# Optimization experiments

Measured on AMD Instinct MI355X. Metric: run time of the kernel, lower is better.

## Reference

```python
import jax, jax.numpy as jnp
import numpy as np
import math

H, E, HD = 12, 768, 64   # heads, embed_dim, per-head hidden
B, S, L = 8, 512, 512    # batch, dec len, enc len
EPS = 1e-12


def layer_norm(x, w, b):
    u = jnp.mean(x, axis=-1, keepdims=True)
    s = jnp.mean((x - u) ** 2, axis=-1, keepdims=True)
    return w * (x - u) / jnp.sqrt(s + EPS) + b


def gelu(x):
    return x * 0.5 * (1.0 + jax.lax.erf(x / math.sqrt(2.0)))


def attention(k, q, w_k, w_q, pw, pb, mask):
    # k:[b,kl,E] q:[b,ql,E] w_k/w_q:[H,E,HD] mask broadcastable to [b,H,ql,kl]
    kx = jnp.einsum('ble,hed->bhld', k, w_k)
    qx = jnp.einsum('bqe,hed->bhqd', q, w_q)
    score = jnp.einsum('bhqd,bhkd->bhqk', qx, kx) / math.sqrt(HD)
    score = jnp.where(mask, score, jnp.asarray(-1e4, score.dtype))
    attn = jax.nn.softmax(score, axis=-1)
    out = jnp.einsum('bhqk,bhkd->bhqd', attn, kx)  # values are kx (as in source)
    b_, h, ql, d = out.shape
    out = out.transpose(0, 2, 1, 3).reshape(b_, ql, h * d)
    return out @ pw + pb


def setup_inputs() -> dict:
    key = jax.random.key(0)
    ks = jax.random.split(key, 16)
    xav = lambda k, shp, fan: jax.random.normal(k, shp, jnp.float32) * math.sqrt(2.0 / fan)
    inp = {
        'X': jax.random.normal(ks[0], (B, S, E), jnp.float32),
        'enc_outputs': jax.random.normal(ks[1], (B, L, E), jnp.float32),
        'enc_valid_lens': jax.random.randint(ks[2], (B,), 1, L + 1, jnp.int32),
        'w_kx1': xav(ks[3], (H, E, HD), E + HD),
        'w_qx1': xav(ks[4], (H, E, HD), E + HD),
        'proj1_w': xav(ks[5], (H * HD, E), 2 * E),
        'proj1_b': jnp.zeros((E,), jnp.float32),
        'ln1_w': jnp.ones((E,), jnp.float32),
        'ln1_b': jnp.zeros((E,), jnp.float32),
        'w_kx2': xav(ks[6], (H, E, HD), E + HD),
        'w_qx2': xav(ks[7], (H, E, HD), E + HD),
        'proj2_w': xav(ks[8], (H * HD, E), 2 * E),
        'proj2_b': jnp.zeros((E,), jnp.float32),
        'ln2_w': jnp.ones((E,), jnp.float32),
        'ln2_b': jnp.zeros((E,), jnp.float32),
        'ffn_w1': xav(ks[9], (E, E), 2 * E),
        'ffn_b1': jnp.zeros((E,), jnp.float32),
        'ffn_w2': xav(ks[10], (E, E), 2 * E),
        'ffn_b2': jnp.zeros((E,), jnp.float32),
        'ln3_w': jnp.ones((E,), jnp.float32),
        'ln3_b': jnp.zeros((E,), jnp.float32),
    }
    return inp


def reference(X, enc_outputs, enc_valid_lens,
              w_kx1, w_qx1, proj1_w, proj1_b, ln1_w, ln1_b,
              w_kx2, w_qx2, proj2_w, proj2_b, ln2_w, ln2_b,
              ffn_w1, ffn_b1, ffn_w2, ffn_b2, ln3_w, ln3_b):
    s = X.shape[1]
    # training path: dec_valid_lens is 2D -> causal mask in Attention
    causal = jnp.tril(jnp.ones((s, s), dtype=bool))[None, None]          # [1,1,s,s]
    X2 = attention(X, X, w_kx1, w_qx1, proj1_w, proj1_b, causal)
    Y = layer_norm(X2 + X, ln1_w, ln1_b)
    # cross mask: key padding from enc_valid_lens (1D branch)
    kl = enc_outputs.shape[1]
    pad = (jnp.arange(kl)[None] < enc_valid_lens[:, None])[:, None, None]  # [b,1,1,kl]
    Y2 = attention(enc_outputs, Y, w_kx2, w_qx2, proj2_w, proj2_b, pad)
    Z = layer_norm(Y2 + Y, ln2_w, ln2_b)
    F = gelu(Z @ ffn_w1 + ffn_b1) @ ffn_w2 + ffn_b2
    return layer_norm(F + Z, ln3_w, ln3_b)
```

## Files before the change

kernel.cpp:

```cpp
#include <hip/hip_runtime.h>
#include <hip/hip_bf16.h>

typedef __hip_bfloat16 bf16;
typedef __attribute__((ext_vector_type(8))) short s8v;
typedef __attribute__((ext_vector_type(4))) short s4v;
typedef __attribute__((ext_vector_type(4))) float f4v;

#define H_ 12
#define E_ 768
#define HD_ 64
#define B_ 8
#define S_ 512
#define M_ 4096

struct P9 { const void* s[8]; bf16* d[8]; const void* vs[10]; bf16* vd[10]; };

typedef __attribute__((address_space(3))) void lds_void;
typedef const __attribute__((address_space(1))) void g_void;

__device__ __forceinline__ void async_copy16(const bf16* g, short* l) {
    __builtin_amdgcn_global_load_lds((g_void*)g, (lds_void*)l, 16, 0, 0);
}

__device__ __forceinline__ float sh2f(short v) {
    unsigned int u = ((unsigned int)(unsigned short)v) << 16;
    return __uint_as_float(u);
}

__device__ __forceinline__ short f2sh(float v) {
    bf16 b = __float2bfloat16(v);
    return *(short*)&b;
}

__device__ __forceinline__ int detect_fp32(const unsigned int* __restrict__ Xh,
                                           int tid, int* scratch) {
    unsigned e = (Xh[tid] >> 7) & 0xFFu;
    int good = (e >= 100u && e <= 141u) ? 1 : 0;
    #pragma unroll
    for (int off = 1; off < 64; off <<= 1) good += __shfl_xor(good, off);
    if ((tid & 63) == 0) scratch[tid >> 6] = good;
    __syncthreads();
    int total = scratch[0] + scratch[1] + scratch[2] + scratch[3];
    return (total <= 154) ? 1 : 0;
}

__device__ __forceinline__ bf16 ldcvt(const void* s, int i, int fp32) {
    return fp32 ? __float2bfloat16(((const float*)s)[i]) : ((const bf16*)s)[i];
}

__global__ __launch_bounds__(256) void prep_kernel(const void* X, const void* enc,
                                                   bf16* Xc, bf16* ENCc,
                                                   P9 p) {
    __shared__ int dsc[4];
    __shared__ float t[64][65];
    const int tid = threadIdx.x;
    const int fp32 = detect_fp32((const unsigned int*)X, tid, dsc);
    const int id = blockIdx.x;

    if (id < 6144) {
        const void* s = (id < 3072) ? X : enc;
        bf16* d = (id < 3072) ? Xc : ENCc;
        int cid = (id < 3072) ? id : id - 3072;
        int i = (cid * 256 + tid) * 4;
        if (fp32) {
            float4 v = *(const float4*)((const float*)s + i);
            bf16 a = __float2bfloat16(v.x), b = __float2bfloat16(v.y),
                 c = __float2bfloat16(v.z), e = __float2bfloat16(v.w);
            s4v o = { *(short*)&a, *(short*)&b, *(short*)&c, *(short*)&e };
            *(s4v*)(d + i) = o;
        } else {
            *(s4v*)(d + i) = *(const s4v*)((const bf16*)s + i);
        }
        return;
    }

    int id2 = id - 6144;
    const int z = id2 / 144;
    const int rem = id2 % 144;
    const int bx = rem % 12, by = rem / 12;

    if (z == 8) {
        int vid = by * 12 + bx;
        if (vid < 10) {
            const void* s = p.vs[vid];
            bf16* d = p.vd[vid];
            for (int i = tid; i < E_; i += 256) d[i] = ldcvt(s, i, fp32);
        }
        return;
    }
    const int c = tid & 63, r0 = tid >> 6;
    if (z < 4) {
        const void* s = p.s[z];
        bf16* d = p.d[z];
        const int e0 = bx * 64, h = by;
        #pragma unroll
        for (int j = 0; j < 16; ++j) {
            int r = r0 * 16 + j;
            int idx = (h * E_ + e0 + r) * HD_ + c;
            t[r][c] = fp32 ? ((const float*)s)[idx] : __bfloat162float(((const bf16*)s)[idx]);
        }
        __syncthreads();
        #pragma unroll
        for (int j = 0; j < 16; ++j) {
            int r = r0 * 16 + j;
            d[(size_t)(h * 64 + r) * E_ + e0 + c] = __float2bfloat16(t[c][r]);
        }
    } else {
        const void* s = p.s[z];
        bf16* d = p.d[z];
        const int k0 = bx * 64, n0 = by * 64;
        #pragma unroll
        for (int j = 0; j < 16; ++j) {
            int r = r0 * 16 + j;
            int idx = (k0 + r) * E_ + n0 + c;
            t[r][c] = fp32 ? ((const float*)s)[idx] : __bfloat162float(((const bf16*)s)[idx]);
        }
        __syncthreads();
        #pragma unroll
        for (int j = 0; j < 16; ++j) {
            int r = r0 * 16 + j;
            d[(size_t)(n0 + r) * E_ + k0 + c] = __float2bfloat16(t[c][r]);
        }
    }
}

template <int EPI>
__global__ __launch_bounds__(256, 4) void gemm3(const bf16* __restrict__ A,
                                                const bf16* __restrict__ Bt,
                                                bf16* __restrict__ C,
                                                const bf16* __restrict__ bias,
                                                const bf16* __restrict__ res) {
    __shared__ short As[64 * 128];
    __shared__ short Bs[64 * 128];
    const int bm = blockIdx.x, bn = blockIdx.y;
    const int tid = threadIdx.x;
    const int w = tid >> 6, l = tid & 63;
    const int wr = (w >> 1) * 32, wc = (w & 1) * 32;
    const int lc = l & 15, quad = l >> 4;
    const int srA = l >> 4, slot = l & 15;

    f4v acc[2][2] = {};

    for (int k0 = 0; k0 < E_; k0 += 128) {
        #pragma unroll
        for (int c = 0; c < 4; ++c) {
            int seg = w * 4 + c;
            int row = seg * 4 + srA;
            int kc = (slot ^ (row & 15)) * 8;
            async_copy16(A + (size_t)(bm * 64 + row) * E_ + k0 + kc, &As[seg * 512]);
            async_copy16(Bt + (size_t)(bn * 64 + row) * E_ + k0 + kc, &Bs[seg * 512]);
        }
        __syncthreads();

        #pragma unroll
        for (int kk = 0; kk < 4; ++kk) {
            s8v a[2], b[2];
            #pragma unroll
            for (int t = 0; t < 2; ++t) {
                int ar = wr + t * 16 + lc;
                a[t] = *(const s8v*)&As[ar * 128 + (((kk * 4 + quad) ^ (ar & 15)) * 8)];
                int bc = wc + t * 16 + lc;
                b[t] = *(const s8v*)&Bs[bc * 128 + (((kk * 4 + quad) ^ (bc & 15)) * 8)];
            }
            acc[0][0] = __builtin_amdgcn_mfma_f32_16x16x32_bf16(a[0], b[0], acc[0][0], 0, 0, 0);
            acc[0][1] = __builtin_amdgcn_mfma_f32_16x16x32_bf16(a[0], b[1], acc[0][1], 0, 0, 0);
            acc[1][0] = __builtin_amdgcn_mfma_f32_16x16x32_bf16(a[1], b[0], acc[1][0], 0, 0, 0);
            acc[1][1] = __builtin_amdgcn_mfma_f32_16x16x32_bf16(a[1], b[1], acc[1][1], 0, 0, 0);
        }
        __syncthreads();
    }

    #pragma unroll
    for (int mt = 0; mt < 2; ++mt)
        #pragma unroll
        for (int nt = 0; nt < 2; ++nt)
            #pragma unroll
            for (int i = 0; i < 4; ++i) {
                int row = bm * 64 + wr + mt * 16 + quad * 4 + i;
                int col = bn * 64 + wc + nt * 16 + lc;
                float v = acc[mt][nt][i];
                if (EPI == 1)
                    v += __bfloat162float(bias[col]) + __bfloat162float(res[(size_t)row * E_ + col]);
                if (EPI == 2) {
                    v += __bfloat162float(bias[col]);
                    v = 0.5f * v * (1.0f + erff(v * 0.70710678118654752f));
                }
                C[(size_t)row * E_ + col] = __float2bfloat16(v);
            }
}

__global__ __launch_bounds__(256, 4) void gemm3q(const bf16* __restrict__ Xc,
                                                 const bf16* __restrict__ ENCc,
                                                 const bf16* __restrict__ Bt,
                                                 bf16* __restrict__ K1,
                                                 bf16* __restrict__ Q1,
                                                 bf16* __restrict__ K2,
                                                 bf16* __restrict__ KT1,
                                                 bf16* __restrict__ KT2) {
    __shared__ short sm[16384];
    short* As = sm;
    short* Bs = sm + 8192;
    const int bm = blockIdx.x, bn = blockIdx.y;
    const int tid = threadIdx.x;
    const int w = tid >> 6, l = tid & 63;
    const int wr = (w >> 1) * 32, wc = (w & 1) * 32;
    const int lc = l & 15, quad = l >> 4;
    const int srA = l >> 4, slot = l & 15;

    const bf16* A = (bn >= 24) ? ENCc : Xc;

    f4v acc[2][2] = {};

    for (int k0 = 0; k0 < E_; k0 += 128) {
        #pragma unroll
        for (int c = 0; c < 4; ++c) {
            int seg = w * 4 + c;
            int row = seg * 4 + srA;
            int kc = (slot ^ (row & 15)) * 8;
            async_copy16(A + (size_t)(bm * 64 + row) * E_ + k0 + kc, &As[seg * 512]);
            async_copy16(Bt + (size_t)(bn * 64 + row) * E_ + k0 + kc, &Bs[seg * 512]);
        }
        __syncthreads();

        #pragma unroll
        for (int kk = 0; kk < 4; ++kk) {
            s8v a[2], b[2];
            #pragma unroll
            for (int t = 0; t < 2; ++t) {
                int ar = wr + t * 16 + lc;
                a[t] = *(const s8v*)&As[ar * 128 + (((kk * 4 + quad) ^ (ar & 15)) * 8)];
                int bc = wc + t * 16 + lc;
                b[t] = *(const s8v*)&Bs[bc * 128 + (((kk * 4 + quad) ^ (bc & 15)) * 8)];
            }
            acc[0][0] = __builtin_amdgcn_mfma_f32_16x16x32_bf16(a[0], b[0], acc[0][0], 0, 0, 0);
            acc[0][1] = __builtin_amdgcn_mfma_f32_16x16x32_bf16(a[0], b[1], acc[0][1], 0, 0, 0);
            acc[1][0] = __builtin_amdgcn_mfma_f32_16x16x32_bf16(a[1], b[0], acc[1][0], 0, 0, 0);
            acc[1][1] = __builtin_amdgcn_mfma_f32_16x16x32_bf16(a[1], b[1], acc[1][1], 0, 0, 0);
        }
        __syncthreads();
    }

    const int band = (bn < 12) ? 0 : (bn < 24) ? 1 : 2;
    const int nb = bn - band * 12;
    bf16* C = (band == 0) ? K1 : (band == 1) ? Q1 : K2;

    #pragma unroll
    for (int mt = 0; mt < 2; ++mt)
        #pragma unroll
        for (int nt = 0; nt < 2; ++nt)
            #pragma unroll
            for (int i = 0; i < 4; ++i) {
                int row = bm * 64 + wr + mt * 16 + quad * 4 + i;
                int col = nb * 64 + wc + nt * 16 + lc;
                C[(size_t)row * E_ + col] = __float2bfloat16(acc[mt][nt][i]);
            }

    if (band != 1) {
        bf16* KT = (band == 0) ? KT1 : KT2;
        #pragma unroll
        for (int mt = 0; mt < 2; ++mt)
            #pragma unroll
            for (int nt = 0; nt < 2; ++nt)
                #pragma unroll
                for (int i = 0; i < 4; ++i) {
                    int srow = wr + mt * 16 + quad * 4 + i;
                    int d = wc + nt * 16 + lc;
                    sm[d * 72 + srow] = f2sh(acc[mt][nt][i]);
                }
        __syncthreads();
        const int drow = tid >> 2, c0 = (tid & 3) * 16;
        s8v o0 = *(const s8v*)&sm[drow * 72 + c0];
        s8v o1 = *(const s8v*)&sm[drow * 72 + c0 + 8];
        const int b = bm >> 3, s0 = (bm & 7) * 64;
        bf16* dp = KT + ((size_t)((b * H_ + nb) * 64 + drow) * S_) + s0 + c0;
        *(s8v*)dp = o0;
        *(s8v*)(dp + 8) = o1;
    }
}

template <bool CAUSAL, bool INLQ>
__global__ __launch_bounds__(256) void attn_kernel(const bf16* __restrict__ Q,
                                                   const bf16* __restrict__ Wq,
                                                   const bf16* __restrict__ Kx,
                                                   const bf16* __restrict__ KT,
                                                   bf16* __restrict__ O,
                                                   const int* __restrict__ vlen) {
    __shared__ short qs[64 * 64];
    __shared__ short ks[64 * 64];
    __shared__ short kts[80 * 64];
    __shared__ short ps[64 * 72];

    const int bh = blockIdx.x, qt = blockIdx.y;
    const int h = bh % H_, b = bh / H_;
    const int tid = threadIdx.x, w = tid >> 6, l = tid & 63;
    const int lr = (l >> 4) * 4, lc = l & 15, quad = l >> 4;
    const int srA = l >> 3, slot = l & 7;
    const int kc = (slot ^ srA) * 8;
    const int rq = w * 16 + lc;

    {
        int r = 64 + (tid >> 4);
        int c4 = (tid & 15) * 4;
        s4v v = {};
        if (r == 64) { v[0] = 0x3F80; v[1] = 0x3F80; v[2] = 0x3F80; v[3] = 0x3F80; }
        *(s4v*)&kts[r * 64 + c4] = v;
    }

    if (INLQ) {
        const int wr = (w >> 1) * 32, wc = (w & 1) * 32;
        const bf16* Arow = Q + (size_t)(b * S_ + qt * 64) * E_;
        const bf16* Brow = Wq + (size_t)(h * 64) * E_;
        f4v qacc[2][2] = {};
        for (int k0 = 0; k0 < E_; k0 += 64) {
            #pragma unroll
            for (int c = 0; c < 2; ++c) {
                int seg = w * 2 + c;
                int row = seg * 8 + srA;
                async_copy16(Arow + (size_t)row * E_ + k0 + kc, &ks[seg * 512]);
                async_copy16(Brow + (size_t)row * E_ + k0 + kc, &kts[seg * 512]);
            }
            __syncthreads();
            #pragma unroll
            for (int kk = 0; kk < 2; ++kk) {
                s8v a[2], bb[2];
                #pragma unroll
                for (int t = 0; t < 2; ++t) {
                    int ar = wr + t * 16 + lc;
                    a[t] = *(const s8v*)&ks[ar * 64 + (((kk * 4 + quad) ^ (ar & 7)) * 8)];
                    int bc = wc + t * 16 + lc;
                    bb[t] = *(const s8v*)&kts[bc * 64 + (((kk * 4 + quad) ^ (bc & 7)) * 8)];
                }
                qacc[0][0] = __builtin_amdgcn_mfma_f32_16x16x32_bf16(a[0], bb[0], qacc[0][0], 0, 0, 0);
                qacc[0][1] = __builtin_amdgcn_mfma_f32_16x16x32_bf16(a[0], bb[1], qacc[0][1], 0, 0, 0);
                qacc[1][0] = __builtin_amdgcn_mfma_f32_16x16x32_bf16(a[1], bb[0], qacc[1][0], 0, 0, 0);
                qacc[1][1] = __builtin_amdgcn_mfma_f32_16x16x32_bf16(a[1], bb[1], qacc[1][1], 0, 0, 0);
            }
            __syncthreads();
        }
        #pragma unroll
        for (int mt = 0; mt < 2; ++mt)
            #pragma unroll
            for (int nt = 0; nt < 2; ++nt)
                #pragma unroll
                for (int i = 0; i < 4; ++i) {
                    int row = wr + mt * 16 + quad * 4 + i;
                    int d = wc + nt * 16 + lc;
                    qs[row * 64 + (((d >> 3) ^ (row & 7)) * 8) + (d & 7)] = f2sh(qacc[mt][nt][i]);
                }
        __syncthreads();
    } else {
        #pragma unroll
        for (int c = 0; c < 2; ++c) {
            int seg = w * 2 + c;
            int row = seg * 8 + srA;
            async_copy16(Q + ((size_t)(b * S_ + qt * 64 + row) * H_ + h) * HD_ + kc, &qs[seg * 512]);
        }
    }

    const int valid = CAUSAL ? S_ : vlen[b];
    const int kmax = CAUSAL ? (qt + 1) : ((valid + 63) >> 6);

    f4v o_acc[5] = {};
    s8v aq0, aq1;

    for (int kt = 0; kt < kmax; ++kt) {
        #pragma unroll
        for (int c = 0; c < 2; ++c) {
            int seg = w * 2 + c;
            int row = seg * 8 + srA;
            async_copy16(Kx + ((size_t)(b * S_ + kt * 64 + row) * H_ + h) * HD_ + kc, &ks[seg * 512]);
            async_copy16(KT + (size_t)(bh * 64 + row) * S_ + kt * 64 + kc, &kts[seg * 512]);
        }
        __syncthreads();

        if (kt == 0) {
            aq0 = *(const s8v*)&qs[rq * 64 + ((quad ^ (rq & 7)) * 8)];
            aq1 = *(const s8v*)&qs[rq * 64 + (((4 + quad) ^ (rq & 7)) * 8)];
        }

        f4v sacc[4] = {};
        #pragma unroll
        for (int nt = 0; nt < 4; nt++) {
            int rk = nt * 16 + lc;
            s8v bk0 = *(const s8v*)&ks[rk * 64 + ((quad ^ (rk & 7)) * 8)];
            s8v bk1 = *(const s8v*)&ks[rk * 64 + (((4 + quad) ^ (rk & 7)) * 8)];
            sacc[nt] = __builtin_amdgcn_mfma_f32_16x16x32_bf16(aq0, bk0, sacc[nt], 0, 0, 0);
            sacc[nt] = __builtin_amdgcn_mfma_f32_16x16x32_bf16(aq1, bk1, sacc[nt], 0, 0, 0);
        }

        #pragma unroll
        for (int i = 0; i < 4; i++) {
            int qabs = qt * 64 + w * 16 + lr + i;
            #pragma unroll
            for (int nt = 0; nt < 4; nt++) {
                int kabs = kt * 64 + nt * 16 + lc;
                bool ok = CAUSAL ? (kabs <= qabs) : (kabs < valid);
                float sv = ok ? fminf(sacc[nt][i] * 0.125f - 20.0f, 0.0f) : -1.0e4f;
                ps[(w * 16 + lr + i) * 72 + nt * 16 + lc] = f2sh(__expf(sv));
            }
        }

        s8v ap0 = *(const s8v*)&ps[rq * 72 + quad * 8];
        s8v ap1 = *(const s8v*)&ps[rq * 72 + 32 + quad * 8];
        #pragma unroll
        for (int dt = 0; dt < 5; dt++) {
            int rd = dt * 16 + lc;
            s8v bv0 = *(const s8v*)&kts[rd * 64 + ((quad ^ (rd & 7)) * 8)];
            s8v bv1 = *(const s8v*)&kts[rd * 64 + (((4 + quad) ^ (rd & 7)) * 8)];
            o_acc[dt] = __builtin_amdgcn_mfma_f32_16x16x32_bf16(ap0, bv0, o_acc[dt], 0, 0, 0);
            o_acc[dt] = __builtin_amdgcn_mfma_f32_16x16x32_bf16(ap1, bv1, o_acc[dt], 0, 0, 0);
        }
        if (kt + 1 < kmax) __syncthreads();
    }

    float li[4];
    #pragma unroll
    for (int i = 0; i < 4; i++) li[i] = __shfl(o_acc[4][i], (l & 48));

    #pragma unroll
    for (int dt = 0; dt < 4; dt++)
        #pragma unroll
        for (int i = 0; i < 4; i++) {
            int q = qt * 64 + w * 16 + lr + i;
            int d = dt * 16 + lc;
            float v = o_acc[dt][i] / li[i];
            O[((size_t)(b * S_ + q) * H_ + h) * HD_ + d] = __float2bfloat16(v);
        }
}

__global__ __launch_bounds__(256) void ln2_kernel(const bf16* __restrict__ X,
                                                  const bf16* __restrict__ wv,
                                                  const bf16* __restrict__ bv,
                                                  bf16* __restrict__ outb,
                                                  float* __restrict__ outf,
                                                  const unsigned int* __restrict__ Xhead) {
    __shared__ int dsc[4];
    int f32out = 0;
    if (outf != nullptr)
        f32out = detect_fp32(Xhead, threadIdx.x, dsc);
    const int row = blockIdx.x * 4 + (threadIdx.x >> 6);
    const int l = threadIdx.x & 63;
    const bf16* xr = X + (size_t)row * E_;
    s8v v8 = *(const s8v*)(xr + l * 8);
    s4v v4 = *(const s4v*)(xr + 512 + l * 4);
    float x[12];
    #pragma unroll
    for (int j = 0; j < 8; ++j) x[j] = sh2f(v8[j]);
    #pragma unroll
    for (int j = 0; j < 4; ++j) x[8 + j] = sh2f(v4[j]);
    float s = 0.f, ss = 0.f;
    #pragma unroll
    for (int j = 0; j < 12; ++j) { s += x[j]; ss += x[j] * x[j]; }
    #pragma unroll
    for (int off = 1; off < 64; off <<= 1) {
        s += __shfl_xor(s, off);
        ss += __shfl_xor(ss, off);
    }
    float mu = s * (1.0f / E_);
    float var = ss * (1.0f / E_) - mu * mu;
    float rstd = rsqrtf(fmaxf(var, 0.0f) + 1e-12f);
    #pragma unroll
    for (int j = 0; j < 12; ++j) {
        int c = (j < 8) ? (l * 8 + j) : (512 + l * 4 + (j - 8));
        float v = (x[j] - mu) * rstd * __bfloat162float(wv[c]) + __bfloat162float(bv[c]);
        if (f32out) outf[(size_t)row * E_ + c] = v;
        else        outb[(size_t)row * E_ + c] = __float2bfloat16(v);
    }
}

extern "C" void kernel_launch(void* const* d_in, const int* in_sizes, int n_in,
                              void* d_out, int out_size, void* d_ws, size_t ws_size,
                              hipStream_t stream) {
    const void* X = d_in[0];
    const void* enc = d_in[1];
    const int* vlen = (const int*)d_in[2];

    char* ws = (char*)d_ws;
    bf16* vecs = (bf16*)(ws + 256);
    char* wbase = ws + 16384;
    const size_t WSZ = (size_t)E_ * E_ * sizeof(bf16);
    bf16* wk1 = (bf16*)(wbase + 0 * WSZ);
    bf16* wq1 = (bf16*)(wbase + 1 * WSZ);
    bf16* wk2 = (bf16*)(wbase + 2 * WSZ);
    bf16* wq2 = (bf16*)(wbase + 3 * WSZ);
    bf16* p1t = (bf16*)(wbase + 4 * WSZ);
    bf16* p2t = (bf16*)(wbase + 5 * WSZ);
    bf16* f1t = (bf16*)(wbase + 6 * WSZ);
    bf16* f2t = (bf16*)(wbase + 7 * WSZ);
    const size_t ASZ = (size_t)M_ * E_ * sizeof(bf16);
    char* abase = wbase + 8 * WSZ;
    bf16* Xc   = (bf16*)(abase + 0 * ASZ);
    bf16* ENCc = (bf16*)(abase + 1 * ASZ);
    bf16* A0  = (bf16*)(abase + 2 * ASZ);
    bf16* A1  = (bf16*)(abase + 3 * ASZ);
    bf16* A2  = (bf16*)(abase + 4 * ASZ);
    bf16* A3  = (bf16*)(abase + 5 * ASZ);
    bf16* A4  = (bf16*)(abase + 6 * ASZ);
    bf16* A5  = (bf16*)(abase + 7 * ASZ);
    bf16* KT1 = (bf16*)(abase + 8 * ASZ);
    bf16* KT2 = (bf16*)(abase + 9 * ASZ);

    bf16* bias1 = vecs + 0 * E_;
    bf16* lw1   = vecs + 1 * E_;
    bf16* lb1   = vecs + 2 * E_;
    bf16* bias2 = vecs + 3 * E_;
    bf16* lw2   = vecs + 4 * E_;
    bf16* lb2   = vecs + 5 * E_;
    bf16* fb1   = vecs + 6 * E_;
    bf16* fb2   = vecs + 7 * E_;
    bf16* lw3   = vecs + 8 * E_;
    bf16* lb3   = vecs + 9 * E_;

    P9 rp;
    rp.s[0] = d_in[3];  rp.d[0] = wk1;
    rp.s[1] = d_in[4];  rp.d[1] = wq1;
    rp.s[2] = d_in[9];  rp.d[2] = wk2;
    rp.s[3] = d_in[10]; rp.d[3] = wq2;
    rp.s[4] = d_in[5];  rp.d[4] = p1t;
    rp.s[5] = d_in[11]; rp.d[5] = p2t;
    rp.s[6] = d_in[15]; rp.d[6] = f1t;
    rp.s[7] = d_in[17]; rp.d[7] = f2t;
    rp.vs[0] = d_in[6];  rp.vd[0] = bias1;
    rp.vs[1] = d_in[7];  rp.vd[1] = lw1;
    rp.vs[2] = d_in[8];  rp.vd[2] = lb1;
    rp.vs[3] = d_in[12]; rp.vd[3] = bias2;
    rp.vs[4] = d_in[13]; rp.vd[4] = lw2;
    rp.vs[5] = d_in[14]; rp.vd[5] = lb2;
    rp.vs[6] = d_in[16]; rp.vd[6] = fb1;
    rp.vs[7] = d_in[18]; rp.vd[7] = fb2;
    rp.vs[8] = d_in[19]; rp.vd[8] = lw3;
    rp.vs[9] = d_in[20]; rp.vd[9] = lb3;

    prep_kernel<<<7440, 256, 0, stream>>>(X, enc, Xc, ENCc, rp);

    gemm3q<<<dim3(64, 36), 256, 0, stream>>>(Xc, ENCc, wk1, A0, A1, A4, KT1, KT2);

    attn_kernel<true, false><<<dim3(96, 8), 256, 0, stream>>>(A1, nullptr, A0, KT1, A2, nullptr);
    gemm3<1><<<dim3(64, 12), 256, 0, stream>>>(A2, p1t, A3, bias1, Xc);
    ln2_kernel<<<M_ / 4, 256, 0, stream>>>(A3, lw1, lb1, A5, nullptr, nullptr);

    attn_kernel<false, true><<<dim3(96, 8), 256, 0, stream>>>(A5, wq2, A4, KT2, A2, vlen);
    gemm3<1><<<dim3(64, 12), 256, 0, stream>>>(A2, p2t, A3, bias2, A5);
    ln2_kernel<<<M_ / 4, 256, 0, stream>>>(A3, lw2, lb2, A0, nullptr, nullptr);

    gemm3<2><<<dim3(64, 12), 256, 0, stream>>>(A0, f1t, A1, fb1, nullptr);
    gemm3<1><<<dim3(64, 12), 256, 0, stream>>>(A1, f2t, A2, fb2, A0);
    ln2_kernel<<<M_ / 4, 256, 0, stream>>>(A2, lw3, lb3, (bf16*)d_out, (float*)d_out,
                                           (const unsigned int*)X);
}
```

Before: 261.0 us.

## Fuse LayerNorm into residual GEMM via last-block atomic counter

Replaces the three separate LayerNorm kernels with a fused GEMM variant. After writing its output tile, each block increments a per-row-tile atomic counter, and the last of the 12 column blocks for that row stripe normalises the 64 full rows. Counters are zeroed in the prep kernel. This removes three kernel launches and a separate pass. In exchange, the LayerNorm runs on only 64 blocks with serialised row loops at the tail, and it adds fence and atomic overhead.

```diff
diff --git a/kernel.cpp b/kernel.cpp
--- a/kernel.cpp
+++ b/kernel.cpp
@@ -13,7 +13,7 @@
 #define S_ 512
 #define M_ 4096
 
-struct P9 { const void* s[8]; bf16* d[8]; const void* vs[10]; bf16* vd[10]; };
+struct P9 { const void* s[8]; bf16* d[8]; const void* vs[10]; bf16* vd[10]; int* cnt; };
 
 typedef __attribute__((address_space(3))) void lds_void;
 typedef const __attribute__((address_space(1))) void g_void;
@@ -85,6 +85,8 @@
             const void* s = p.vs[vid];
             bf16* d = p.vd[vid];
             for (int i = tid; i < E_; i += 256) d[i] = ldcvt(s, i, fp32);
+        } else if (vid == 10) {
+            if (tid < 192) p.cnt[tid] = 0;
         }
         return;
     }
@@ -187,6 +189,116 @@
                 }
                 C[(size_t)row * E_ + col] = __float2bfloat16(v);
             }
+}
+
+template <int DET>
+__global__ __launch_bounds__(256, 4) void gemm3ln(const bf16* __restrict__ A,
+                                                  const bf16* __restrict__ Bt,
+                                                  bf16* __restrict__ C,
+                                                  const bf16* __restrict__ bias,
+                                                  const bf16* __restrict__ res,
+                                                  const bf16* __restrict__ lnw,
+                                                  const bf16* __restrict__ lnb,
+                                                  bf16* __restrict__ outb,
+                                                  float* __restrict__ outf,
+                                                  int* __restrict__ cnt,
+                                                  const unsigned int* __restrict__ Xhead) {
+    __shared__ short As[64 * 128];
+    __shared__ short Bs[64 * 128];
+    __shared__ int dsc[4];
+    __shared__ int lastFlag;
+    const int bm = blockIdx.x, bn = blockIdx.y;
+    const int tid = threadIdx.x;
+    const int w = tid >> 6, l = tid & 63;
+    const int wr = (w >> 1) * 32, wc = (w & 1) * 32;
+    const int lc = l & 15, quad = l >> 4;
+    const int srA = l >> 4, slot = l & 15;
+
+    f4v acc[2][2] = {};
+
+    for (int k0 = 0; k0 < E_; k0 += 128) {
+        #pragma unroll
+        for (int c = 0; c < 4; ++c) {
+            int seg = w * 4 + c;
+            int row = seg * 4 + srA;
+            int kc = (slot ^ (row & 15)) * 8;
+            async_copy16(A + (size_t)(bm * 64 + row) * E_ + k0 + kc, &As[seg * 512]);
+            async_copy16(Bt + (size_t)(bn * 64 + row) * E_ + k0 + kc, &Bs[seg * 512]);
+        }
+        __syncthreads();
+
+        #pragma unroll
+        for (int kk = 0; kk < 4; ++kk) {
+            s8v a[2], b[2];
+            #pragma unroll
+            for (int t = 0; t < 2; ++t) {
+                int ar = wr + t * 16 + lc;
+                a[t] = *(const s8v*)&As[ar * 128 + (((kk * 4 + quad) ^ (ar & 15)) * 8)];
+                int bc = wc + t * 16 + lc;
+                b[t] = *(const s8v*)&Bs[bc * 128 + (((kk * 4 + quad) ^ (bc & 15)) * 8)];
+            }
+            acc[0][0] = __builtin_amdgcn_mfma_f32_16x16x32_bf16(a[0], b[0], acc[0][0], 0, 0, 0);
+            acc[0][1] = __builtin_amdgcn_mfma_f32_16x16x32_bf16(a[0], b[1], acc[0][1], 0, 0, 0);
+            acc[1][0] = __builtin_amdgcn_mfma_f32_16x16x32_bf16(a[1], b[0], acc[1][0], 0, 0, 0);
+            acc[1][1] = __builtin_amdgcn_mfma_f32_16x16x32_bf16(a[1], b[1], acc[1][1], 0, 0, 0);
+        }
+        __syncthreads();
+    }
+
+    #pragma unroll
+    for (int mt = 0; mt < 2; ++mt)
+        #pragma unroll
+        for (int nt = 0; nt < 2; ++nt)
+            #pragma unroll
+            for (int i = 0; i < 4; ++i) {
+                int row = bm * 64 + wr + mt * 16 + quad * 4 + i;
+                int col = bn * 64 + wc + nt * 16 + lc;
+                float v = acc[mt][nt][i]
+                        + __bfloat162float(bias[col])
+                        + __bfloat162float(res[(size_t)row * E_ + col]);
+                C[(size_t)row * E_ + col] = __float2bfloat16(v);
+            }
+
+    __threadfence();
+    __syncthreads();
+    if (tid == 0) lastFlag = (atomicAdd(cnt + bm, 1) == 11);
+    __syncthreads();
+    if (!lastFlag) return;
+    __threadfence();
+
+    int f32o = 0;
+    if (DET) f32o = detect_fp32(Xhead, tid, dsc);
+
+    #pragma unroll 1
+    for (int rr = 0; rr < 16; ++rr) {
+        int row = bm * 64 + w * 16 + rr;
+        const bf16* xr = C + (size_t)row * E_;
+        s8v v8 = *(const s8v*)(xr + l * 8);
+        s4v v4 = *(const s4v*)(xr + 512 + l * 4);
+        float x[12];
+        #pragma unroll
+        for (int j = 0; j < 8; ++j) x[j] = sh2f(v8[j]);
+        #pragma unroll
+        for (int j = 0; j < 4; ++j) x[8 + j] = sh2f(v4[j]);
+        float s = 0.f, ss = 0.f;
+        #pragma unroll
+        for (int j = 0; j < 12; ++j) { s += x[j]; ss += x[j] * x[j]; }
+        #pragma unroll
+        for (int off = 1; off < 64; off <<= 1) {
+            s += __shfl_xor(s, off);
+            ss += __shfl_xor(ss, off);
+        }
+        float mu = s * (1.0f / E_);
+        float var = ss * (1.0f / E_) - mu * mu;
+        float rstd = rsqrtf(fmaxf(var, 0.0f) + 1e-12f);
+        #pragma unroll
+        for (int j = 0; j < 12; ++j) {
+            int c = (j < 8) ? (l * 8 + j) : (512 + l * 4 + (j - 8));
+            float v = (x[j] - mu) * rstd * __bfloat162float(lnw[c]) + __bfloat162float(lnb[c]);
+            if (DET && f32o) outf[(size_t)row * E_ + c] = v;
+            else             outb[(size_t)row * E_ + c] = __float2bfloat16(v);
+        }
+    }
 }
 
 __global__ __launch_bounds__(256, 4) void gemm3q(const bf16* __restrict__ Xc,
@@ -428,46 +540,6 @@
         }
 }
 
-__global__ __launch_bounds__(256) void ln2_kernel(const bf16* __restrict__ X,
-                                                  const bf16* __restrict__ wv,
-                                                  const bf16* __restrict__ bv,
-                                                  bf16* __restrict__ outb,
-                                                  float* __restrict__ outf,
-                                                  const unsigned int* __restrict__ Xhead) {
-    __shared__ int dsc[4];
-    int f32out = 0;
-    if (outf != nullptr)
-        f32out = detect_fp32(Xhead, threadIdx.x, dsc);
-    const int row = blockIdx.x * 4 + (threadIdx.x >> 6);
-    const int l = threadIdx.x & 63;
-    const bf16* xr = X + (size_t)row * E_;
-    s8v v8 = *(const s8v*)(xr + l * 8);
-    s4v v4 = *(const s4v*)(xr + 512 + l * 4);
-    float x[12];
-    #pragma unroll
-    for (int j = 0; j < 8; ++j) x[j] = sh2f(v8[j]);
-    #pragma unroll
-    for (int j = 0; j < 4; ++j) x[8 + j] = sh2f(v4[j]);
-    float s = 0.f, ss = 0.f;
-    #pragma unroll
-    for (int j = 0; j < 12; ++j) { s += x[j]; ss += x[j] * x[j]; }
-    #pragma unroll
-    for (int off = 1; off < 64; off <<= 1) {
-        s += __shfl_xor(s, off);
-        ss += __shfl_xor(ss, off);
-    }
-    float mu = s * (1.0f / E_);
-    float var = ss * (1.0f / E_) - mu * mu;
-    float rstd = rsqrtf(fmaxf(var, 0.0f) + 1e-12f);
-    #pragma unroll
-    for (int j = 0; j < 12; ++j) {
-        int c = (j < 8) ? (l * 8 + j) : (512 + l * 4 + (j - 8));
-        float v = (x[j] - mu) * rstd * __bfloat162float(wv[c]) + __bfloat162float(bv[c]);
-        if (f32out) outf[(size_t)row * E_ + c] = v;
-        else        outb[(size_t)row * E_ + c] = __float2bfloat16(v);
-    }
-}
-
 extern "C" void kernel_launch(void* const* d_in, const int* in_sizes, int n_in,
                               void* d_out, int out_size, void* d_ws, size_t ws_size,
                               hipStream_t stream) {
@@ -476,7 +548,8 @@
     const int* vlen = (const int*)d_in[2];
 
     char* ws = (char*)d_ws;
-    bf16* vecs = (bf16*)(ws + 256);
+    int* cnt = (int*)ws;
+    bf16* vecs = (bf16*)(ws + 1024);
     char* wbase = ws + 16384;
     const size_t WSZ = (size_t)E_ * E_ * sizeof(bf16);
     bf16* wk1 = (bf16*)(wbase + 0 * WSZ);
@@ -530,21 +603,22 @@
     rp.vs[7] = d_in[18]; rp.vd[7] = fb2;
     rp.vs[8] = d_in[19]; rp.vd[8] = lw3;
     rp.vs[9] = d_in[20]; rp.vd[9] = lb3;
+    rp.cnt = cnt;
 
     prep_kernel<<<7440, 256, 0, stream>>>(X, enc, Xc, ENCc, rp);
 
     gemm3q<<<dim3(64, 36), 256, 0, stream>>>(Xc, ENCc, wk1, A0, A1, A4, KT1, KT2);
 
     attn_kernel<true, false><<<dim3(96, 8), 256, 0, stream>>>(A1, nullptr, A0, KT1, A2, nullptr);
-    gemm3<1><<<dim3(64, 12), 256, 0, stream>>>(A2, p1t, A3, bias1, Xc);
-    ln2_kernel<<<M_ / 4, 256, 0, stream>>>(A3, lw1, lb1, A5, nullptr, nullptr);
+    gemm3ln<0><<<dim3(64, 12), 256, 0, stream>>>(A2, p1t, A3, bias1, Xc,
+                                                 lw1, lb1, A5, nullptr, cnt + 0, nullptr);
 
     attn_kernel<false, true><<<dim3(96, 8), 256, 0, stream>>>(A5, wq2, A4, KT2, A2, vlen);
-    gemm3<1><<<dim3(64, 12), 256, 0, stream>>>(A2, p2t, A3, bias2, A5);
-    ln2_kernel<<<M_ / 4, 256, 0, stream>>>(A3, lw2, lb2, A0, nullptr, nullptr);
+    gemm3ln<0><<<dim3(64, 12), 256, 0, stream>>>(A2, p2t, A3, bias2, A5,
+                                                 lw2, lb2, A0, nullptr, cnt + 64, nullptr);
 
     gemm3<2><<<dim3(64, 12), 256, 0, stream>>>(A0, f1t, A1, fb1, nullptr);
-    gemm3<1><<<dim3(64, 12), 256, 0, stream>>>(A1, f2t, A2, fb2, A0);
-    ln2_kernel<<<M_ / 4, 256, 0, stream>>>(A2, lw3, lb3, (bf16*)d_out, (float*)d_out,
-                                           (const unsigned int*)X);
-}
+    gemm3ln<1><<<dim3(64, 12), 256, 0, stream>>>(A1, f2t, A2, fb2, A0,
+                                                 lw3, lb3, (bf16*)d_out, (float*)d_out,
+                                                 cnt + 128, (const unsigned int*)X);
+}
```

Result: slower. 564.5 us (+116.3%).

## Double-buffer QKV projection GEMM and rebalance causal attention block schedule

Applied to the files above, without the earlier changes.

The fused K/Q projection GEMM now uses 64-wide K tiles in two LDS buffers, issuing async loads for the next tile while MFMAs run on the current one, instead of loading a 128-wide tile then waiting. The causal attention kernel remaps block IDs through a lookup table that interleaves long and short query tiles across heads, so concurrently resident blocks carry more even causal work. This adds table logic and depends on the grid shape matching the 96x8 layout.

```diff
diff --git a/kernel.cpp b/kernel.cpp
--- a/kernel.cpp
+++ b/kernel.cpp
@@ -198,39 +198,52 @@
                                                  bf16* __restrict__ KT1,
                                                  bf16* __restrict__ KT2) {
     __shared__ short sm[16384];
-    short* As = sm;
-    short* Bs = sm + 8192;
     const int bm = blockIdx.x, bn = blockIdx.y;
     const int tid = threadIdx.x;
     const int w = tid >> 6, l = tid & 63;
     const int wr = (w >> 1) * 32, wc = (w & 1) * 32;
     const int lc = l & 15, quad = l >> 4;
-    const int srA = l >> 4, slot = l & 15;
+    const int srA = l >> 3, slot = l & 7;
+    const int kc = (slot ^ srA) * 8;
 
     const bf16* A = (bn >= 24) ? ENCc : Xc;
+    const bf16* Ab = A + (size_t)(bm * 64) * E_;
+    const bf16* Bb = Bt + (size_t)(bn * 64) * E_;
 
     f4v acc[2][2] = {};
 
-    for (int k0 = 0; k0 < E_; k0 += 128) {
-        #pragma unroll
-        for (int c = 0; c < 4; ++c) {
-            int seg = w * 4 + c;
-            int row = seg * 4 + srA;
-            int kc = (slot ^ (row & 15)) * 8;
-            async_copy16(A + (size_t)(bm * 64 + row) * E_ + k0 + kc, &As[seg * 512]);
-            async_copy16(Bt + (size_t)(bn * 64 + row) * E_ + k0 + kc, &Bs[seg * 512]);
-        }
-        __syncthreads();
-
-        #pragma unroll
-        for (int kk = 0; kk < 4; ++kk) {
+    #pragma unroll
+    for (int c = 0; c < 2; ++c) {
+        int seg = w * 2 + c;
+        int row = seg * 8 + srA;
+        async_copy16(Ab + (size_t)row * E_ + kc, &sm[seg * 512]);
+        async_copy16(Bb + (size_t)row * E_ + kc, &sm[8192 + seg * 512]);
+    }
+    __syncthreads();
+
+    #pragma unroll
+    for (int kt = 0; kt < 12; ++kt) {
+        const int cur = (kt & 1) * 4096;
+        if (kt < 11) {
+            const int nxt = ((kt + 1) & 1) * 4096;
+            const int k0 = (kt + 1) * 64;
+            #pragma unroll
+            for (int c = 0; c < 2; ++c) {
+                int seg = w * 2 + c;
+                int row = seg * 8 + srA;
+                async_copy16(Ab + (size_t)row * E_ + k0 + kc, &sm[nxt + seg * 512]);
+                async_copy16(Bb + (size_t)row * E_ + k0 + kc, &sm[8192 + nxt + seg * 512]);
+            }
+        }
+        #pragma unroll
+        for (int kk = 0; kk < 2; ++kk) {
             s8v a[2], b[2];
             #pragma unroll
             for (int t = 0; t < 2; ++t) {
                 int ar = wr + t * 16 + lc;
-                a[t] = *(const s8v*)&As[ar * 128 + (((kk * 4 + quad) ^ (ar & 15)) * 8)];
+                a[t] = *(const s8v*)&sm[cur + ar * 64 + (((kk * 4 + quad) ^ (ar & 7)) * 8)];
                 int bc = wc + t * 16 + lc;
-                b[t] = *(const s8v*)&Bs[bc * 128 + (((kk * 4 + quad) ^ (bc & 15)) * 8)];
+                b[t] = *(const s8v*)&sm[8192 + cur + bc * 64 + (((kk * 4 + quad) ^ (bc & 7)) * 8)];
             }
             acc[0][0] = __builtin_amdgcn_mfma_f32_16x16x32_bf16(a[0], b[0], acc[0][0], 0, 0, 0);
             acc[0][1] = __builtin_amdgcn_mfma_f32_16x16x32_bf16(a[0], b[1], acc[0][1], 0, 0, 0);
@@ -290,7 +303,20 @@
     __shared__ short kts[80 * 64];
     __shared__ short ps[64 * 72];
 
-    const int bh = blockIdx.x, qt = blockIdx.y;
+    int bh, qt;
+    if (CAUSAL) {
+        const signed char Tq[8][3] = {{7,3,0},{7,3,1},{7,4,0},{6,4,1},
+                                      {6,4,0},{6,3,1},{5,5,2},{5,2,2}};
+        const signed char To[8][3] = {{0,0,0},{1,1,0},{2,0,1},{0,1,1},
+                                      {1,2,2},{2,2,2},{0,1,0},{2,1,2}};
+        const int id = blockIdx.y * 96 + blockIdx.x;
+        const int s = id & 255, j = id >> 8, r = s & 7;
+        qt = Tq[r][j];
+        bh = (s >> 3) * 3 + To[r][j];
+    } else {
+        bh = blockIdx.x;
+        qt = blockIdx.y;
+    }
     const int h = bh % H_, b = bh / H_;
     const int tid = threadIdx.x, w = tid >> 6, l = tid & 63;
     const int lr = (l >> 4) * 4, lc = l & 15, quad = l >> 4;
```

Result: no change. 259.3 us (-0.7%).
